# Optimization experiments

Hardware: AMD Instinct MI355X
Metric: run time of the kernel (lower is better)

Reference implementation:

```python
import jax, jax.numpy as jnp
import numpy as np

NU = 500000   # num_users
NI = 500000   # num_items
E = 128       # embedding_dim
F = 172       # feature_dim
B = 65536     # number of events in the batch
MSG = 2 * E + F  # GRU input dim = 428


def _gru_cell(x, h, wih, whh, bih, bhh):
    # PyTorch GRUCell: gates ordered (r, z, n)
    gi = x @ wih.T + bih            # [B, 3E]
    gh = h @ whh.T + bhh            # [B, 3E]
    ir, iz, in_ = jnp.split(gi, 3, axis=-1)
    hr, hz, hn = jnp.split(gh, 3, axis=-1)
    r = jax.nn.sigmoid(ir + hr)
    z = jax.nn.sigmoid(iz + hz)
    n = jnp.tanh(in_ + r * hn)
    return (1.0 - z) * n + z * h


def setup_inputs() -> dict:
    key = jax.random.key(0)
    ks = jax.random.split(key, 18)
    s = 0.05  # init scale ~ 1/sqrt(E)
    return {
        "user_ids": jax.random.randint(ks[0], (B,), 0, NU),
        "item_ids": jax.random.randint(ks[1], (B,), 0, NI),
        "timestamps": jax.random.uniform(ks[2], (B,), dtype=jnp.float32) * 1000.0,
        "features": jax.random.normal(ks[3], (B, F), dtype=jnp.float32),
        "query_time": 1200,
        "memory": jax.random.normal(ks[4], (NU + NI, E), dtype=jnp.float32) * 0.1,
        "last_time": jax.random.uniform(ks[5], (NU + NI,), dtype=jnp.float32) * 1000.0,
        "time_w": jax.random.normal(ks[6], (E,), dtype=jnp.float32) * 0.01,  # Linear(1,E,bias=False)
        "u_wih": jax.random.normal(ks[7], (3 * E, MSG), dtype=jnp.float32) * s,
        "u_whh": jax.random.normal(ks[8], (3 * E, E), dtype=jnp.float32) * s,
        "u_bih": jax.random.normal(ks[9], (3 * E,), dtype=jnp.float32) * s,
        "u_bhh": jax.random.normal(ks[10], (3 * E,), dtype=jnp.float32) * s,
        "i_wih": jax.random.normal(ks[11], (3 * E, MSG), dtype=jnp.float32) * s,
        "i_whh": jax.random.normal(ks[12], (3 * E, E), dtype=jnp.float32) * s,
        "i_bih": jax.random.normal(ks[13], (3 * E,), dtype=jnp.float32) * s,
        "i_bhh": jax.random.normal(ks[14], (3 * E,), dtype=jnp.float32) * s,
        "gate_w": jax.random.normal(ks[15], (E, 2 * E), dtype=jnp.float32) * s,
        "gate_b": jnp.zeros((E,), dtype=jnp.float32),
        "pred_w": jax.random.normal(ks[16], (E, E), dtype=jnp.float32) * s,
        "pred_b": jnp.zeros((E,), dtype=jnp.float32),
    }


def reference(user_ids, item_ids, timestamps, features, query_time, memory, last_time,
              time_w, u_wih, u_whh, u_bih, u_bhh, i_wih, i_whh, i_bih, i_bhh,
              gate_w, gate_b, pred_w, pred_b):
    item_nodes = item_ids + NU  # offset items into global node id space
    # per-event gather from node memory
    old_user = memory[user_ids]          # [B, E]
    old_item = memory[item_nodes]        # [B, E]
    last_u = last_time[user_ids]         # [B]
    last_i = last_time[item_nodes]       # [B]

    du = (timestamps - last_u)[:, None]  # [B, 1]
    di = (timestamps - last_i)[:, None]
    # time projection: emb * (1 + Linear(dt))
    proj_user = old_user * (1.0 + du * time_w)
    proj_item = old_item * (1.0 + di * time_w)

    d_query = (jnp.float32(query_time) - last_u)[:, None]
    query_user = old_user * (1.0 + d_query * time_w)

    # peer message mode: user_msg = proj_item, item_msg = proj_user
    user_input = jnp.concatenate([proj_user, proj_item, features], axis=-1)  # [B, MSG]
    item_input = jnp.concatenate([proj_item, proj_user, features], axis=-1)

    new_user = _gru_cell(user_input, old_user, u_wih, u_whh, u_bih, u_bhh)
    new_item = _gru_cell(item_input, old_item, i_wih, i_whh, i_bih, i_bhh)

    # memory gate: g*new + (1-g)*old
    gu = jax.nn.sigmoid(jnp.concatenate([old_user, new_user], axis=-1) @ gate_w.T + gate_b)
    gi = jax.nn.sigmoid(jnp.concatenate([old_item, new_item], axis=-1) @ gate_w.T + gate_b)
    new_user = gu * new_user + (1.0 - gu) * old_user
    new_item = gi * new_item + (1.0 - gi) * old_item

    pred_item_emb = query_user @ pred_w.T + pred_b
    return (pred_item_emb, new_user, new_item)
```

## Files before the change

kernel.cpp:

```cpp
#include <hip/hip_runtime.h>
#include <cstdint>
#include <cstddef>

#define CNU 500000
#define CB  65536
#define CE  128
#define CF  172
#define EV  32

typedef unsigned short ushort_t;
typedef __attribute__((ext_vector_type(8))) short b8;
typedef __attribute__((ext_vector_type(4))) short b4;
typedef __attribute__((ext_vector_type(4))) float f4;

#define MFMA16(a,b,c) __builtin_amdgcn_mfma_f32_16x16x32_bf16((a),(b),(c),0,0,0)

#define FRAG 512
#define U_KT 18
#define U_NT 24
#define U_SZ (U_NT*U_KT*FRAG)
#define PU_OFF 0
#define PI_OFF U_SZ
#define PG_OFF (2*U_SZ)
#define G_SZ (8*8*FRAG)
#define PP_OFF (PG_OFF + G_SZ)
#define P_SZ (8*4*FRAG)

#define SWZ(r, c) ((c) ^ (((r) & 7) << 3))
#define AFRAG(T, r, c) (*(const b8*)&(T)[(r)][SWZ((r), (c))])

__device__ __forceinline__ ushort_t f2bf(float f) {
  unsigned u = __float_as_uint(f);
  return (ushort_t)((u + 0x7FFFu + ((u >> 16) & 1u)) >> 16);
}
__device__ __forceinline__ float bf2f(ushort_t h) {
  return __uint_as_float(((unsigned)h) << 16);
}
__device__ __forceinline__ float sigmoid_(float x) { return 1.0f/(1.0f+__expf(-x)); }
__device__ __forceinline__ float tanh_(float x) { float e=__expf(2.0f*x); return 1.0f-2.0f/(e+1.0f); }

struct __align__(16) SLds {
  ushort_t PU[EV][128];
  ushort_t PI[EV][128];
  ushort_t FE[EV][192];
  ushort_t OU[EV][128];
  ushort_t OI[EV][128];
  ushort_t HU[EV][128];
  ushort_t HI[EV][128];
  ushort_t QU[EV][128];
};

extern "C" __global__ void prep_weights(
    const float* __restrict__ u_wih, const float* __restrict__ u_whh,
    const float* __restrict__ i_wih, const float* __restrict__ i_whh,
    const float* __restrict__ gate_w, const float* __restrict__ pred_w,
    ushort_t* __restrict__ ws)
{
  const int stride = gridDim.x * blockDim.x;
  const int tid = blockIdx.x * blockDim.x + threadIdx.x;
  for (int i = tid; i < U_SZ; i += stride) {
    const int nt = i / (U_KT*FRAG);
    const int r1 = i - nt*(U_KT*FRAG);
    const int kt = r1 / FRAG;
    const int e  = r1 - kt*FRAG;
    const int l  = e >> 3, j = e & 7;
    const int n  = nt*16 + (l & 15);
    const int k  = (l >> 4)*8 + j;
    float vu, vi;
    if (kt < 14) {
      const int kk = kt*32 + k;
      vu = (kk < 428) ? u_wih[(size_t)n*428 + kk] : 0.0f;
      vi = (kk < 428) ? i_wih[(size_t)n*428 + kk] : 0.0f;
    } else {
      const int kk = (kt - 14)*32 + k;
      vu = u_whh[(size_t)n*128 + kk];
      vi = i_whh[(size_t)n*128 + kk];
    }
    ws[PU_OFF + i] = f2bf(vu);
    ws[PI_OFF + i] = f2bf(vi);
  }
  for (int i = tid; i < G_SZ; i += stride) {
    const int nt = i / (8*FRAG);
    const int r1 = i - nt*(8*FRAG);
    const int kt = r1 / FRAG;
    const int e  = r1 - kt*FRAG;
    const int l  = e >> 3, j = e & 7;
    const int n  = nt*16 + (l & 15);
    const int kk = kt*32 + (l >> 4)*8 + j;
    ws[PG_OFF + i] = f2bf(gate_w[(size_t)n*256 + kk]);
  }
  for (int i = tid; i < P_SZ; i += stride) {
    const int nt = i / (4*FRAG);
    const int r1 = i - nt*(4*FRAG);
    const int kt = r1 / FRAG;
    const int e  = r1 - kt*FRAG;
    const int l  = e >> 3, j = e & 7;
    const int n  = nt*16 + (l & 15);
    const int kk = kt*32 + (l >> 4)*8 + j;
    ws[PP_OFF + i] = f2bf(pred_w[(size_t)n*128 + kk]);
  }
}

extern "C" __global__ void __launch_bounds__(512, 4)
jodie_main(const int* __restrict__ user_ids, const int* __restrict__ item_ids,
           const float* __restrict__ timestamps, const float* __restrict__ features,
           const int* __restrict__ query_time, const float* __restrict__ memv,
           const float* __restrict__ last_time, const float* __restrict__ time_w,
           const float* __restrict__ u_bih, const float* __restrict__ u_bhh,
           const float* __restrict__ i_bih, const float* __restrict__ i_bhh,
           const float* __restrict__ gate_b, const float* __restrict__ pred_b,
           const ushort_t* __restrict__ ws, float* __restrict__ d_out)
{
  __shared__ SLds s;
  const int t  = threadIdx.x;
  const int e0 = blockIdx.x * EV;

  {
    const int e  = t >> 4;
    const int c8 = (t & 15) * 8;
    const int ge = e0 + e;
    const int u   = user_ids[ge];
    const int itn = item_ids[ge] + CNU;
    const float ts = timestamps[ge];
    const float lu = last_time[u];
    const float li = last_time[itn];
    const float qt = (float)query_time[0];
    const float du = ts - lu, di = ts - li, dq = qt - lu;

    const float4 tw0 = *(const float4*)&time_w[c8];
    const float4 tw1 = *(const float4*)&time_w[c8 + 4];
    const float4 ou0 = *(const float4*)&memv[(size_t)u  *CE + c8];
    const float4 ou1 = *(const float4*)&memv[(size_t)u  *CE + c8 + 4];
    const float4 oi0 = *(const float4*)&memv[(size_t)itn*CE + c8];
    const float4 oi1 = *(const float4*)&memv[(size_t)itn*CE + c8 + 4];
    const float twv[8] = {tw0.x,tw0.y,tw0.z,tw0.w, tw1.x,tw1.y,tw1.z,tw1.w};
    const float ouv[8] = {ou0.x,ou0.y,ou0.z,ou0.w, ou1.x,ou1.y,ou1.z,ou1.w};
    const float oiv[8] = {oi0.x,oi0.y,oi0.z,oi0.w, oi1.x,oi1.y,oi1.z,oi1.w};

    union { ushort_t u[8]; b8 v; } xu, xi, hu, hi, qv;
#pragma unroll
    for (int j = 0; j < 8; ++j) {
      xu.u[j] = f2bf(ouv[j] * (1.0f + du*twv[j]));
      xi.u[j] = f2bf(oiv[j] * (1.0f + di*twv[j]));
      hu.u[j] = f2bf(ouv[j]);
      hi.u[j] = f2bf(oiv[j]);
      qv.u[j] = f2bf(ouv[j] * (1.0f + dq*twv[j]));
    }
    *(b8*)&s.PU[e][SWZ(e, c8)] = xu.v;
    *(b8*)&s.PI[e][SWZ(e, c8)] = xi.v;
    *(b8*)&s.OU[e][SWZ(e, c8)] = hu.v;
    *(b8*)&s.OI[e][SWZ(e, c8)] = hi.v;
    *(b8*)&s.QU[e][SWZ(e, c8)] = qv.v;
  }
  for (int i = t; i < EV*43; i += 512) {
    const int e = i / 43, q = i - e*43;
    const float4 fv = *(const float4*)&features[(size_t)(e0 + e)*CF + q*4];
    union { ushort_t u[4]; b4 v; } fb;
    fb.u[0] = f2bf(fv.x); fb.u[1] = f2bf(fv.y);
    fb.u[2] = f2bf(fv.z); fb.u[3] = f2bf(fv.w);
    *(b4*)&s.FE[e][SWZ(e, q*4)] = fb.v;
  }
  for (int i = t; i < EV*20; i += 512) {
    const int e = i / 20, c = 172 + (i - e*20);
    s.FE[e][SWZ(e, c)] = 0;
  }
  __syncthreads();

  const int wv   = t >> 6, l = t & 63;
  const int lrow = l & 15;
  const int lk   = (l >> 4) * 8;
  const int col  = wv*16 + lrow;

  const float bru = u_bih[col]     + u_bhh[col];
  const float bzu = u_bih[col+128] + u_bhh[col+128];
  const float bnu = u_bih[col+256];
  const float bhu = u_bhh[col+256];
  const float bri = i_bih[col]     + i_bhh[col];
  const float bzi = i_bih[col+128] + i_bhh[col+128];
  const float bni = i_bih[col+256];
  const float bhi = i_bhh[col+256];

  f4 aru[2], azu[2], anu[2], ari[2], azi[2], ani[2];
#pragma unroll
  for (int m = 0; m < 2; ++m) {
    aru[m] = (f4){bru,bru,bru,bru};  azu[m] = (f4){bzu,bzu,bzu,bzu};
    anu[m] = (f4){bnu,bnu,bnu,bnu};  ari[m] = (f4){bri,bri,bri,bri};
    azi[m] = (f4){bzi,bzi,bzi,bzi};  ani[m] = (f4){bni,bni,bni,bni};
  }

  const ushort_t* Wru = ws + PU_OFF + (size_t)(wv     )*U_KT*FRAG + l*8;
  const ushort_t* Wzu = ws + PU_OFF + (size_t)(wv +  8)*U_KT*FRAG + l*8;
  const ushort_t* Wnu = ws + PU_OFF + (size_t)(wv + 16)*U_KT*FRAG + l*8;
  const ushort_t* Wri = ws + PI_OFF + (size_t)(wv     )*U_KT*FRAG + l*8;
  const ushort_t* Wzi = ws + PI_OFF + (size_t)(wv +  8)*U_KT*FRAG + l*8;
  const ushort_t* Wni = ws + PI_OFF + (size_t)(wv + 16)*U_KT*FRAG + l*8;

#pragma unroll
  for (int pf = 0; pf < 14; ++pf) {
    const int kti = (pf < 4) ? pf + 4 : (pf < 8) ? pf - 4 : pf;
    b8 a0, a1;
    if (pf < 4)       { a0 = AFRAG(s.PU, lrow, 32*pf + lk);     a1 = AFRAG(s.PU, 16+lrow, 32*pf + lk); }
    else if (pf < 8)  { a0 = AFRAG(s.PI, lrow, 32*(pf-4) + lk); a1 = AFRAG(s.PI, 16+lrow, 32*(pf-4) + lk); }
    else              { a0 = AFRAG(s.FE, lrow, 32*(pf-8) + lk); a1 = AFRAG(s.FE, 16+lrow, 32*(pf-8) + lk); }
    b8 fru = *(const b8*)(Wru + (size_t)pf*FRAG);
    b8 fzu = *(const b8*)(Wzu + (size_t)pf*FRAG);
    b8 fnu = *(const b8*)(Wnu + (size_t)pf*FRAG);
    b8 fri = *(const b8*)(Wri + (size_t)kti*FRAG);
    b8 fzi = *(const b8*)(Wzi + (size_t)kti*FRAG);
    b8 fni = *(const b8*)(Wni + (size_t)kti*FRAG);
    aru[0] = MFMA16(a0, fru, aru[0]);  aru[1] = MFMA16(a1, fru, aru[1]);
    azu[0] = MFMA16(a0, fzu, azu[0]);  azu[1] = MFMA16(a1, fzu, azu[1]);
    anu[0] = MFMA16(a0, fnu, anu[0]);  anu[1] = MFMA16(a1, fnu, anu[1]);
    ari[0] = MFMA16(a0, fri, ari[0]);  ari[1] = MFMA16(a1, fri, ari[1]);
    azi[0] = MFMA16(a0, fzi, azi[0]);  azi[1] = MFMA16(a1, fzi, azi[1]);
    ani[0] = MFMA16(a0, fni, ani[0]);  ani[1] = MFMA16(a1, fni, ani[1]);
  }

  {
    f4 ah[2];
    ah[0] = (f4){bhu,bhu,bhu,bhu}; ah[1] = ah[0];
#pragma unroll
    for (int kt = 0; kt < 4; ++kt) {
      b8 h0 = AFRAG(s.OU, lrow, 32*kt + lk);
      b8 h1 = AFRAG(s.OU, 16+lrow, 32*kt + lk);
      b8 fr = *(const b8*)(Wru + (size_t)(14+kt)*FRAG);
      b8 fz = *(const b8*)(Wzu + (size_t)(14+kt)*FRAG);
      b8 fn = *(const b8*)(Wnu + (size_t)(14+kt)*FRAG);
      aru[0] = MFMA16(h0, fr, aru[0]);  aru[1] = MFMA16(h1, fr, aru[1]);
      azu[0] = MFMA16(h0, fz, azu[0]);  azu[1] = MFMA16(h1, fz, azu[1]);
      ah[0]  = MFMA16(h0, fn, ah[0]);   ah[1]  = MFMA16(h1, fn, ah[1]);
    }
#pragma unroll
    for (int m = 0; m < 2; ++m)
#pragma unroll
      for (int r4 = 0; r4 < 4; ++r4) {
        const int row = m*16 + (l >> 4)*4 + r4;
        const float rr = sigmoid_(aru[m][r4]);
        const float zz = sigmoid_(azu[m][r4]);
        const float nn = tanh_(anu[m][r4] + rr*ah[m][r4]);
        const float h  = bf2f(s.OU[row][SWZ(row, col)]);
        s.HU[row][SWZ(row, col)] = f2bf((1.0f - zz)*nn + zz*h);
      }
  }

  {
    f4 ah[2];
    ah[0] = (f4){bhi,bhi,bhi,bhi}; ah[1] = ah[0];
#pragma unroll
    for (int kt = 0; kt < 4; ++kt) {
      b8 h0 = AFRAG(s.OI, lrow, 32*kt + lk);
      b8 h1 = AFRAG(s.OI, 16+lrow, 32*kt + lk);
      b8 fr = *(const b8*)(Wri + (size_t)(14+kt)*FRAG);
      b8 fz = *(const b8*)(Wzi + (size_t)(14+kt)*FRAG);
      b8 fn = *(const b8*)(Wni + (size_t)(14+kt)*FRAG);
      ari[0] = MFMA16(h0, fr, ari[0]);  ari[1] = MFMA16(h1, fr, ari[1]);
      azi[0] = MFMA16(h0, fz, azi[0]);  azi[1] = MFMA16(h1, fz, azi[1]);
      ah[0]  = MFMA16(h0, fn, ah[0]);   ah[1]  = MFMA16(h1, fn, ah[1]);
    }
#pragma unroll
    for (int m = 0; m < 2; ++m)
#pragma unroll
      for (int r4 = 0; r4 < 4; ++r4) {
        const int row = m*16 + (l >> 4)*4 + r4;
        const float rr = sigmoid_(ari[m][r4]);
        const float zz = sigmoid_(azi[m][r4]);
        const float nn = tanh_(ani[m][r4] + rr*ah[m][r4]);
        const float h  = bf2f(s.OI[row][SWZ(row, col)]);
        s.HI[row][SWZ(row, col)] = f2bf((1.0f - zz)*nn + zz*h);
      }
  }

  {
    const float bp = pred_b[col];
    f4 ap[2];
    ap[0] = (f4){bp,bp,bp,bp}; ap[1] = ap[0];
    const ushort_t* WP = ws + PP_OFF + (size_t)wv*4*FRAG + l*8;
#pragma unroll
    for (int kt = 0; kt < 4; ++kt) {
      b8 a0 = AFRAG(s.QU, lrow, 32*kt + lk);
      b8 a1 = AFRAG(s.QU, 16+lrow, 32*kt + lk);
      b8 fp = *(const b8*)(WP + (size_t)kt*FRAG);
      ap[0] = MFMA16(a0, fp, ap[0]);
      ap[1] = MFMA16(a1, fp, ap[1]);
    }
#pragma unroll
    for (int m = 0; m < 2; ++m)
#pragma unroll
      for (int r4 = 0; r4 < 4; ++r4) {
        const int row = m*16 + (l >> 4)*4 + r4;
        d_out[(size_t)(e0 + row)*CE + col] = ap[m][r4];
      }
  }

  __syncthreads();

  {
    const float gb = gate_b[col];
    f4 agu[2], agi[2];
    agu[0] = (f4){gb,gb,gb,gb};
    agu[1] = agu[0]; agi[0] = agu[0]; agi[1] = agu[0];
    const ushort_t* WG = ws + PG_OFF + (size_t)wv*8*FRAG + l*8;
#pragma unroll
    for (int kt = 0; kt < 8; ++kt) {
      b8 fg = *(const b8*)(WG + (size_t)kt*FRAG);
      b8 au0, au1, ai0, ai1;
      if (kt < 4) {
        au0 = AFRAG(s.OU, lrow, 32*kt + lk);  au1 = AFRAG(s.OU, 16+lrow, 32*kt + lk);
        ai0 = AFRAG(s.OI, lrow, 32*kt + lk);  ai1 = AFRAG(s.OI, 16+lrow, 32*kt + lk);
      } else {
        au0 = AFRAG(s.HU, lrow, 32*(kt-4) + lk);  au1 = AFRAG(s.HU, 16+lrow, 32*(kt-4) + lk);
        ai0 = AFRAG(s.HI, lrow, 32*(kt-4) + lk);  ai1 = AFRAG(s.HI, 16+lrow, 32*(kt-4) + lk);
      }
      agu[0] = MFMA16(au0, fg, agu[0]);
      agu[1] = MFMA16(au1, fg, agu[1]);
      agi[0] = MFMA16(ai0, fg, agi[0]);
      agi[1] = MFMA16(ai1, fg, agi[1]);
    }
    float* __restrict__ outu = d_out + (size_t)CB*CE;
    float* __restrict__ outi = d_out + (size_t)2*CB*CE;
#pragma unroll
    for (int m = 0; m < 2; ++m)
#pragma unroll
      for (int r4 = 0; r4 < 4; ++r4) {
        const int row = m*16 + (l >> 4)*4 + r4;
        const float gu = sigmoid_(agu[m][r4]);
        const float gi = sigmoid_(agi[m][r4]);
        const float hu  = bf2f(s.OU[row][SWZ(row, col)]);
        const float hpu = bf2f(s.HU[row][SWZ(row, col)]);
        const float hi  = bf2f(s.OI[row][SWZ(row, col)]);
        const float hpi = bf2f(s.HI[row][SWZ(row, col)]);
        outu[(size_t)(e0 + row)*CE + col] = gu*hpu + (1.0f - gu)*hu;
        outi[(size_t)(e0 + row)*CE + col] = gi*hpi + (1.0f - gi)*hi;
      }
  }
}

extern "C" void kernel_launch(void* const* d_in, const int* in_sizes, int n_in,
                              void* d_out, int out_size, void* d_ws, size_t ws_size,
                              hipStream_t stream) {
  const int*   user_ids   = (const int*)d_in[0];
  const int*   item_ids   = (const int*)d_in[1];
  const float* timestamps = (const float*)d_in[2];
  const float* features   = (const float*)d_in[3];
  const int*   query_time = (const int*)d_in[4];
  const float* memv       = (const float*)d_in[5];
  const float* last_time  = (const float*)d_in[6];
  const float* time_w     = (const float*)d_in[7];
  const float* u_wih = (const float*)d_in[8];
  const float* u_whh = (const float*)d_in[9];
  const float* u_bih = (const float*)d_in[10];
  const float* u_bhh = (const float*)d_in[11];
  const float* i_wih = (const float*)d_in[12];
  const float* i_whh = (const float*)d_in[13];
  const float* i_bih = (const float*)d_in[14];
  const float* i_bhh = (const float*)d_in[15];
  const float* gate_w = (const float*)d_in[16];
  const float* gate_b = (const float*)d_in[17];
  const float* pred_w = (const float*)d_in[18];
  const float* pred_b = (const float*)d_in[19];
  ushort_t* ws = (ushort_t*)d_ws;
  float* out = (float*)d_out;

  prep_weights<<<dim3(256), dim3(256), 0, stream>>>(u_wih, u_whh, i_wih, i_whh,
                                                    gate_w, pred_w, ws);
  jodie_main<<<dim3(CB/EV), dim3(512), 0, stream>>>(user_ids, item_ids, timestamps,
                                                    features, query_time, memv,
                                                    last_time, time_w,
                                                    u_bih, u_bhh, i_bih, i_bhh,
                                                    gate_b, pred_b, ws, out);
}
```

Before: 146.5 us.

## Double events per block and alias LDS buffers to fit larger tile

Each block now handles 64 events instead of 32, so every bf16 weight fragment loaded from global memory feeds four MFMA row tiles rather than two. This halves weight traffic per event. To keep LDS usage manageable, the prediction matmul runs first so the QU buffer can be reused for the new user hidden state, and PU is reused for the new item hidden state, with extra barriers added. Accumulator register count doubles and launch bounds drop to 2 blocks per SM, which lowers occupancy and latency hiding for the gather loads.

```diff
diff --git a/kernel.cpp b/kernel.cpp
--- a/kernel.cpp
+++ b/kernel.cpp
@@ -6,7 +6,7 @@
 #define CB  65536
 #define CE  128
 #define CF  172
-#define EV  32
+#define EV  64
 
 typedef unsigned short ushort_t;
 typedef __attribute__((ext_vector_type(8))) short b8;
@@ -45,8 +45,6 @@
   ushort_t FE[EV][192];
   ushort_t OU[EV][128];
   ushort_t OI[EV][128];
-  ushort_t HU[EV][128];
-  ushort_t HI[EV][128];
   ushort_t QU[EV][128];
 };
 
@@ -101,7 +99,7 @@
   }
 }
 
-extern "C" __global__ void __launch_bounds__(512, 4)
+extern "C" __global__ void __launch_bounds__(512, 2)
 jodie_main(const int* __restrict__ user_ids, const int* __restrict__ item_ids,
            const float* __restrict__ timestamps, const float* __restrict__ features,
            const int* __restrict__ query_time, const float* __restrict__ memv,
@@ -116,41 +114,44 @@
   const int e0 = blockIdx.x * EV;
 
   {
-    const int e  = t >> 4;
     const int c8 = (t & 15) * 8;
-    const int ge = e0 + e;
-    const int u   = user_ids[ge];
-    const int itn = item_ids[ge] + CNU;
-    const float ts = timestamps[ge];
-    const float lu = last_time[u];
-    const float li = last_time[itn];
     const float qt = (float)query_time[0];
-    const float du = ts - lu, di = ts - li, dq = qt - lu;
-
     const float4 tw0 = *(const float4*)&time_w[c8];
     const float4 tw1 = *(const float4*)&time_w[c8 + 4];
-    const float4 ou0 = *(const float4*)&memv[(size_t)u  *CE + c8];
-    const float4 ou1 = *(const float4*)&memv[(size_t)u  *CE + c8 + 4];
-    const float4 oi0 = *(const float4*)&memv[(size_t)itn*CE + c8];
-    const float4 oi1 = *(const float4*)&memv[(size_t)itn*CE + c8 + 4];
     const float twv[8] = {tw0.x,tw0.y,tw0.z,tw0.w, tw1.x,tw1.y,tw1.z,tw1.w};
-    const float ouv[8] = {ou0.x,ou0.y,ou0.z,ou0.w, ou1.x,ou1.y,ou1.z,ou1.w};
-    const float oiv[8] = {oi0.x,oi0.y,oi0.z,oi0.w, oi1.x,oi1.y,oi1.z,oi1.w};
-
-    union { ushort_t u[8]; b8 v; } xu, xi, hu, hi, qv;
-#pragma unroll
-    for (int j = 0; j < 8; ++j) {
-      xu.u[j] = f2bf(ouv[j] * (1.0f + du*twv[j]));
-      xi.u[j] = f2bf(oiv[j] * (1.0f + di*twv[j]));
-      hu.u[j] = f2bf(ouv[j]);
-      hi.u[j] = f2bf(oiv[j]);
-      qv.u[j] = f2bf(ouv[j] * (1.0f + dq*twv[j]));
-    }
-    *(b8*)&s.PU[e][SWZ(e, c8)] = xu.v;
-    *(b8*)&s.PI[e][SWZ(e, c8)] = xi.v;
-    *(b8*)&s.OU[e][SWZ(e, c8)] = hu.v;
-    *(b8*)&s.OI[e][SWZ(e, c8)] = hi.v;
-    *(b8*)&s.QU[e][SWZ(e, c8)] = qv.v;
+#pragma unroll
+    for (int ep = 0; ep < 2; ++ep) {
+      const int e  = ep*32 + (t >> 4);
+      const int ge = e0 + e;
+      const int u   = user_ids[ge];
+      const int itn = item_ids[ge] + CNU;
+      const float ts = timestamps[ge];
+      const float lu = last_time[u];
+      const float li = last_time[itn];
+      const float du = ts - lu, di = ts - li, dq = qt - lu;
+
+      const float4 ou0 = *(const float4*)&memv[(size_t)u  *CE + c8];
+      const float4 ou1 = *(const float4*)&memv[(size_t)u  *CE + c8 + 4];
+      const float4 oi0 = *(const float4*)&memv[(size_t)itn*CE + c8];
+      const float4 oi1 = *(const float4*)&memv[(size_t)itn*CE + c8 + 4];
+      const float ouv[8] = {ou0.x,ou0.y,ou0.z,ou0.w, ou1.x,ou1.y,ou1.z,ou1.w};
+      const float oiv[8] = {oi0.x,oi0.y,oi0.z,oi0.w, oi1.x,oi1.y,oi1.z,oi1.w};
+
+      union { ushort_t u[8]; b8 v; } xu, xi, hu, hi, qv;
+#pragma unroll
+      for (int j = 0; j < 8; ++j) {
+        xu.u[j] = f2bf(ouv[j] * (1.0f + du*twv[j]));
+        xi.u[j] = f2bf(oiv[j] * (1.0f + di*twv[j]));
+        hu.u[j] = f2bf(ouv[j]);
+        hi.u[j] = f2bf(oiv[j]);
+        qv.u[j] = f2bf(ouv[j] * (1.0f + dq*twv[j]));
+      }
+      *(b8*)&s.PU[e][SWZ(e, c8)] = xu.v;
+      *(b8*)&s.PI[e][SWZ(e, c8)] = xi.v;
+      *(b8*)&s.OU[e][SWZ(e, c8)] = hu.v;
+      *(b8*)&s.OI[e][SWZ(e, c8)] = hi.v;
+      *(b8*)&s.QU[e][SWZ(e, c8)] = qv.v;
+    }
   }
   for (int i = t; i < EV*43; i += 512) {
     const int e = i / 43, q = i - e*43;
@@ -170,6 +171,31 @@
   const int lrow = l & 15;
   const int lk   = (l >> 4) * 8;
   const int col  = wv*16 + lrow;
+
+  {
+    const float bp = pred_b[col];
+    f4 ap[4];
+#pragma unroll
+    for (int m = 0; m < 4; ++m) ap[m] = (f4){bp,bp,bp,bp};
+    const ushort_t* WP = ws + PP_OFF + (size_t)wv*4*FRAG + l*8;
+#pragma unroll
+    for (int kt = 0; kt < 4; ++kt) {
+      b8 fp = *(const b8*)(WP + (size_t)kt*FRAG);
+#pragma unroll
+      for (int m = 0; m < 4; ++m) {
+        b8 a = AFRAG(s.QU, m*16 + lrow, 32*kt + lk);
+        ap[m] = MFMA16(a, fp, ap[m]);
+      }
+    }
+#pragma unroll
+    for (int m = 0; m < 4; ++m)
+#pragma unroll
+      for (int r4 = 0; r4 < 4; ++r4) {
+        const int row = m*16 + (l >> 4)*4 + r4;
+        d_out[(size_t)(e0 + row)*CE + col] = ap[m][r4];
+      }
+  }
+  __syncthreads();
 
   const float bru = u_bih[col]     + u_bhh[col];
   const float bzu = u_bih[col+128] + u_bhh[col+128];
@@ -180,9 +206,9 @@
   const float bni = i_bih[col+256];
   const float bhi = i_bhh[col+256];
 
-  f4 aru[2], azu[2], anu[2], ari[2], azi[2], ani[2];
-#pragma unroll
-  for (int m = 0; m < 2; ++m) {
+  f4 aru[4], azu[4], anu[4], ari[4], azi[4], ani[4];
+#pragma unroll
+  for (int m = 0; m < 4; ++m) {
     aru[m] = (f4){bru,bru,bru,bru};  azu[m] = (f4){bzu,bzu,bzu,bzu};
     anu[m] = (f4){bnu,bnu,bnu,bnu};  ari[m] = (f4){bri,bri,bri,bri};
     azi[m] = (f4){bzi,bzi,bzi,bzi};  ani[m] = (f4){bni,bni,bni,bni};
@@ -195,43 +221,55 @@
   const ushort_t* Wzi = ws + PI_OFF + (size_t)(wv +  8)*U_KT*FRAG + l*8;
   const ushort_t* Wni = ws + PI_OFF + (size_t)(wv + 16)*U_KT*FRAG + l*8;
 
-#pragma unroll
-  for (int pf = 0; pf < 14; ++pf) {
-    const int kti = (pf < 4) ? pf + 4 : (pf < 8) ? pf - 4 : pf;
-    b8 a0, a1;
-    if (pf < 4)       { a0 = AFRAG(s.PU, lrow, 32*pf + lk);     a1 = AFRAG(s.PU, 16+lrow, 32*pf + lk); }
-    else if (pf < 8)  { a0 = AFRAG(s.PI, lrow, 32*(pf-4) + lk); a1 = AFRAG(s.PI, 16+lrow, 32*(pf-4) + lk); }
-    else              { a0 = AFRAG(s.FE, lrow, 32*(pf-8) + lk); a1 = AFRAG(s.FE, 16+lrow, 32*(pf-8) + lk); }
-    b8 fru = *(const b8*)(Wru + (size_t)pf*FRAG);
-    b8 fzu = *(const b8*)(Wzu + (size_t)pf*FRAG);
-    b8 fnu = *(const b8*)(Wnu + (size_t)pf*FRAG);
-    b8 fri = *(const b8*)(Wri + (size_t)kti*FRAG);
-    b8 fzi = *(const b8*)(Wzi + (size_t)kti*FRAG);
-    b8 fni = *(const b8*)(Wni + (size_t)kti*FRAG);
-    aru[0] = MFMA16(a0, fru, aru[0]);  aru[1] = MFMA16(a1, fru, aru[1]);
-    azu[0] = MFMA16(a0, fzu, azu[0]);  azu[1] = MFMA16(a1, fzu, azu[1]);
-    anu[0] = MFMA16(a0, fnu, anu[0]);  anu[1] = MFMA16(a1, fnu, anu[1]);
-    ari[0] = MFMA16(a0, fri, ari[0]);  ari[1] = MFMA16(a1, fri, ari[1]);
-    azi[0] = MFMA16(a0, fzi, azi[0]);  azi[1] = MFMA16(a1, fzi, azi[1]);
-    ani[0] = MFMA16(a0, fni, ani[0]);  ani[1] = MFMA16(a1, fni, ani[1]);
-  }
-
-  {
-    f4 ah[2];
-    ah[0] = (f4){bhu,bhu,bhu,bhu}; ah[1] = ah[0];
+#define GI_STEP(TILE, pf, ktu, kti)                                          \
+  {                                                                          \
+    b8 a_[4];                                                                \
+    _Pragma("unroll")                                                        \
+    for (int m = 0; m < 4; ++m) a_[m] = AFRAG(TILE, m*16 + lrow, 32*(pf) + lk); \
+    b8 fru = *(const b8*)(Wru + (size_t)(ktu)*FRAG);                         \
+    b8 fzu = *(const b8*)(Wzu + (size_t)(ktu)*FRAG);                         \
+    b8 fnu = *(const b8*)(Wnu + (size_t)(ktu)*FRAG);                         \
+    b8 fri = *(const b8*)(Wri + (size_t)(kti)*FRAG);                         \
+    b8 fzi = *(const b8*)(Wzi + (size_t)(kti)*FRAG);                         \
+    b8 fni = *(const b8*)(Wni + (size_t)(kti)*FRAG);                         \
+    _Pragma("unroll")                                                        \
+    for (int m = 0; m < 4; ++m) {                                            \
+      aru[m] = MFMA16(a_[m], fru, aru[m]);                                   \
+      azu[m] = MFMA16(a_[m], fzu, azu[m]);                                   \
+      anu[m] = MFMA16(a_[m], fnu, anu[m]);                                   \
+      ari[m] = MFMA16(a_[m], fri, ari[m]);                                   \
+      azi[m] = MFMA16(a_[m], fzi, azi[m]);                                   \
+      ani[m] = MFMA16(a_[m], fni, ani[m]);                                   \
+    }                                                                        \
+  }
+
+#pragma unroll
+  for (int pf = 0; pf < 4; ++pf) GI_STEP(s.PU, pf, pf, pf + 4)
+#pragma unroll
+  for (int pf = 0; pf < 4; ++pf) GI_STEP(s.PI, pf, pf + 4, pf)
+#pragma unroll
+  for (int pf = 0; pf < 6; ++pf) GI_STEP(s.FE, pf, pf + 8, pf + 8)
+#undef GI_STEP
+
+  {
+    f4 ah[4];
+#pragma unroll
+    for (int m = 0; m < 4; ++m) ah[m] = (f4){bhu,bhu,bhu,bhu};
 #pragma unroll
     for (int kt = 0; kt < 4; ++kt) {
-      b8 h0 = AFRAG(s.OU, lrow, 32*kt + lk);
-      b8 h1 = AFRAG(s.OU, 16+lrow, 32*kt + lk);
       b8 fr = *(const b8*)(Wru + (size_t)(14+kt)*FRAG);
       b8 fz = *(const b8*)(Wzu + (size_t)(14+kt)*FRAG);
       b8 fn = *(const b8*)(Wnu + (size_t)(14+kt)*FRAG);
-      aru[0] = MFMA16(h0, fr, aru[0]);  aru[1] = MFMA16(h1, fr, aru[1]);
-      azu[0] = MFMA16(h0, fz, azu[0]);  azu[1] = MFMA16(h1, fz, azu[1]);
-      ah[0]  = MFMA16(h0, fn, ah[0]);   ah[1]  = MFMA16(h1, fn, ah[1]);
-    }
-#pragma unroll
-    for (int m = 0; m < 2; ++m)
+#pragma unroll
+      for (int m = 0; m < 4; ++m) {
+        b8 h = AFRAG(s.OU, m*16 + lrow, 32*kt + lk);
+        aru[m] = MFMA16(h, fr, aru[m]);
+        azu[m] = MFMA16(h, fz, azu[m]);
+        ah[m]  = MFMA16(h, fn, ah[m]);
+      }
+    }
+#pragma unroll
+    for (int m = 0; m < 4; ++m)
 #pragma unroll
       for (int r4 = 0; r4 < 4; ++r4) {
         const int row = m*16 + (l >> 4)*4 + r4;
@@ -239,26 +277,30 @@
         const float zz = sigmoid_(azu[m][r4]);
         const float nn = tanh_(anu[m][r4] + rr*ah[m][r4]);
         const float h  = bf2f(s.OU[row][SWZ(row, col)]);
-        s.HU[row][SWZ(row, col)] = f2bf((1.0f - zz)*nn + zz*h);
-      }
-  }
-
-  {
-    f4 ah[2];
-    ah[0] = (f4){bhi,bhi,bhi,bhi}; ah[1] = ah[0];
+        s.QU[row][SWZ(row, col)] = f2bf((1.0f - zz)*nn + zz*h);
+      }
+  }
+  __syncthreads();
+
+  {
+    f4 ah[4];
+#pragma unroll
+    for (int m = 0; m < 4; ++m) ah[m] = (f4){bhi,bhi,bhi,bhi};
 #pragma unroll
     for (int kt = 0; kt < 4; ++kt) {
-      b8 h0 = AFRAG(s.OI, lrow, 32*kt + lk);
-      b8 h1 = AFRAG(s.OI, 16+lrow, 32*kt + lk);
       b8 fr = *(const b8*)(Wri + (size_t)(14+kt)*FRAG);
       b8 fz = *(const b8*)(Wzi + (size_t)(14+kt)*FRAG);
       b8 fn = *(const b8*)(Wni + (size_t)(14+kt)*FRAG);
-      ari[0] = MFMA16(h0, fr, ari[0]);  ari[1] = MFMA16(h1, fr, ari[1]);
-      azi[0] = MFMA16(h0, fz, azi[0]);  azi[1] = MFMA16(h1, fz, azi[1]);
-      ah[0]  = MFMA16(h0, fn, ah[0]);   ah[1]  = MFMA16(h1, fn, ah[1]);
-    }
-#pragma unroll
-    for (int m = 0; m < 2; ++m)
+#pragma unroll
+      for (int m = 0; m < 4; ++m) {
+        b8 h = AFRAG(s.OI, m*16 + lrow, 32*kt + lk);
+        ari[m] = MFMA16(h, fr, ari[m]);
+        azi[m] = MFMA16(h, fz, azi[m]);
+        ah[m]  = MFMA16(h, fn, ah[m]);
+      }
+    }
+#pragma unroll
+    for (int m = 0; m < 4; ++m)
 #pragma unroll
       for (int r4 = 0; r4 < 4; ++r4) {
         const int row = m*16 + (l >> 4)*4 + r4;
@@ -266,69 +308,43 @@
         const float zz = sigmoid_(azi[m][r4]);
         const float nn = tanh_(ani[m][r4] + rr*ah[m][r4]);
         const float h  = bf2f(s.OI[row][SWZ(row, col)]);
-        s.HI[row][SWZ(row, col)] = f2bf((1.0f - zz)*nn + zz*h);
-      }
-  }
-
-  {
-    const float bp = pred_b[col];
-    f4 ap[2];
-    ap[0] = (f4){bp,bp,bp,bp}; ap[1] = ap[0];
-    const ushort_t* WP = ws + PP_OFF + (size_t)wv*4*FRAG + l*8;
-#pragma unroll
-    for (int kt = 0; kt < 4; ++kt) {
-      b8 a0 = AFRAG(s.QU, lrow, 32*kt + lk);
-      b8 a1 = AFRAG(s.QU, 16+lrow, 32*kt + lk);
-      b8 fp = *(const b8*)(WP + (size_t)kt*FRAG);
-      ap[0] = MFMA16(a0, fp, ap[0]);
-      ap[1] = MFMA16(a1, fp, ap[1]);
-    }
-#pragma unroll
-    for (int m = 0; m < 2; ++m)
-#pragma unroll
-      for (int r4 = 0; r4 < 4; ++r4) {
-        const int row = m*16 + (l >> 4)*4 + r4;
-        d_out[(size_t)(e0 + row)*CE + col] = ap[m][r4];
-      }
-  }
-
+        s.PU[row][SWZ(row, col)] = f2bf((1.0f - zz)*nn + zz*h);
+      }
+  }
   __syncthreads();
 
   {
     const float gb = gate_b[col];
-    f4 agu[2], agi[2];
-    agu[0] = (f4){gb,gb,gb,gb};
-    agu[1] = agu[0]; agi[0] = agu[0]; agi[1] = agu[0];
+    f4 agu[4], agi[4];
+#pragma unroll
+    for (int m = 0; m < 4; ++m) { agu[m] = (f4){gb,gb,gb,gb}; agi[m] = agu[m]; }
     const ushort_t* WG = ws + PG_OFF + (size_t)wv*8*FRAG + l*8;
 #pragma unroll
     for (int kt = 0; kt < 8; ++kt) {
       b8 fg = *(const b8*)(WG + (size_t)kt*FRAG);
-      b8 au0, au1, ai0, ai1;
-      if (kt < 4) {
-        au0 = AFRAG(s.OU, lrow, 32*kt + lk);  au1 = AFRAG(s.OU, 16+lrow, 32*kt + lk);
-        ai0 = AFRAG(s.OI, lrow, 32*kt + lk);  ai1 = AFRAG(s.OI, 16+lrow, 32*kt + lk);
-      } else {
-        au0 = AFRAG(s.HU, lrow, 32*(kt-4) + lk);  au1 = AFRAG(s.HU, 16+lrow, 32*(kt-4) + lk);
-        ai0 = AFRAG(s.HI, lrow, 32*(kt-4) + lk);  ai1 = AFRAG(s.HI, 16+lrow, 32*(kt-4) + lk);
-      }
-      agu[0] = MFMA16(au0, fg, agu[0]);
-      agu[1] = MFMA16(au1, fg, agu[1]);
-      agi[0] = MFMA16(ai0, fg, agi[0]);
-      agi[1] = MFMA16(ai1, fg, agi[1]);
+#pragma unroll
+      for (int m = 0; m < 4; ++m) {
+        b8 au = (kt < 4) ? AFRAG(s.OU, m*16 + lrow, 32*kt + lk)
+                         : AFRAG(s.QU, m*16 + lrow, 32*(kt-4) + lk);
+        b8 ai = (kt < 4) ? AFRAG(s.OI, m*16 + lrow, 32*kt + lk)
+                         : AFRAG(s.PU, m*16 + lrow, 32*(kt-4) + lk);
+        agu[m] = MFMA16(au, fg, agu[m]);
+        agi[m] = MFMA16(ai, fg, agi[m]);
+      }
     }
     float* __restrict__ outu = d_out + (size_t)CB*CE;
     float* __restrict__ outi = d_out + (size_t)2*CB*CE;
 #pragma unroll
-    for (int m = 0; m < 2; ++m)
+    for (int m = 0; m < 4; ++m)
 #pragma unroll
       for (int r4 = 0; r4 < 4; ++r4) {
         const int row = m*16 + (l >> 4)*4 + r4;
         const float gu = sigmoid_(agu[m][r4]);
         const float gi = sigmoid_(agi[m][r4]);
         const float hu  = bf2f(s.OU[row][SWZ(row, col)]);
-        const float hpu = bf2f(s.HU[row][SWZ(row, col)]);
+        const float hpu = bf2f(s.QU[row][SWZ(row, col)]);
         const float hi  = bf2f(s.OI[row][SWZ(row, col)]);
-        const float hpi = bf2f(s.HI[row][SWZ(row, col)]);
+        const float hpi = bf2f(s.PU[row][SWZ(row, col)]);
         outu[(size_t)(e0 + row)*CE + col] = gu*hpu + (1.0f - gu)*hu;
         outi[(size_t)(e0 + row)*CE + col] = gi*hpi + (1.0f - gi)*hi;
       }
```

Measured after the change: 140.1 us. 1.05x faster.
